# Kernel tuning notes

Measured on AMD Instinct MI355X. Metric: run time of the kernel, lower is better.

The kernel has to match this reference:

```python
import jax, jax.numpy as jnp
import numpy as np

EPS = 0.1          # entropic regularization (init eps)
MAX_ITER = 20      # Sinkhorn iterations (init max_iter)
THRESH = 0.1       # convergence threshold on err (from torch source)
COS_EPS = 1e-8     # CosineSimilarity eps


def setup_inputs() -> dict:
    key = jax.random.key(0)
    kx, ky = jax.random.split(key)
    B, N, M, D = 4, 1024, 1024, 512
    x = jax.random.normal(kx, (B, N, D), dtype=jnp.float32)
    y = jax.random.normal(ky, (B, M, D), dtype=jnp.float32)
    nu = jnp.full((B, M), 1.0 / M, dtype=jnp.float32)  # target marginal
    return {"x": x, "y": y, "nu": nu}


def _cost_matrix(x, y):
    # C_ij = 1 - cos(x_i, y_j), with torch CosineSimilarity eps semantics
    dot = jnp.einsum("bnd,bmd->bnm", x, y)
    nx = jnp.linalg.norm(x, axis=-1)  # [B, N]
    ny = jnp.linalg.norm(y, axis=-1)  # [B, M]
    denom = jnp.maximum(nx[:, :, None] * ny[:, None, :], COS_EPS)
    return 1.0 - dot / denom  # [B, N, M]


def reference(x, y, nu):
    C = _cost_matrix(x, y)  # [B, N, M]
    B, N, _ = C.shape
    log_mu = jnp.log(jnp.full((B, N), 1.0 / N, dtype=C.dtype) + 1e-8)  # [B, N]
    log_nu = jnp.log(nu + 1e-8)  # [B, M]

    def Mmat(u, v):
        # M_ij = (-C_ij + u_i + v_j) / eps
        return (-C + u[:, :, None] + v[:, None, :]) / EPS

    def step(carry, _):
        u, v, done = carry
        u_new = EPS * (log_mu - jax.scipy.special.logsumexp(Mmat(u, v), axis=-1)) + u
        v_new = EPS * (log_nu - jax.scipy.special.logsumexp(Mmat(u_new, v), axis=-2)) + v
        err = jnp.abs(u_new - u).sum(-1).mean()
        # freeze updates after convergence (emulates the host-side break)
        u2 = jnp.where(done, u, u_new)
        v2 = jnp.where(done, v, v_new)
        return (u2, v2, done | (err < THRESH)), None

    u0 = jnp.zeros_like(log_mu)
    v0 = jnp.zeros_like(log_nu)
    (u, v, _), _ = jax.lax.scan(step, (u0, v0, jnp.array(False)), None, length=MAX_ITER)

    pi = jnp.exp(Mmat(u, v))  # transport plan [B, N, M]
    cost = jnp.sum(pi * C, axis=(-2, -1))  # [B]  (reduction='none')
    return cost
```

## Files before the change

### kernel.cpp

```cpp
#include <hip/hip_runtime.h>
#include <math.h>

#define EPS      0.1f
#define INV_EPS  10.0f
#define THRESH   0.1f
#define MAX_IT   20

#define BB 4
#define NN 1024
#define MM 1024
#define DD 512

#define MU_P (1.0f / 1024.0f + 1e-8f)

#define GBLK 128
#define TBLK 512

#define OFF_K    ((size_t)0)
#define OFF_XB   ((size_t)2097152)
#define OFF_YB   ((size_t)3145728)
#define OFF_NX   ((size_t)4194304)
#define OFF_NY   (OFF_NX + 4096)
#define OFF_NUP  (OFF_NY + 4096)
#define OFF_CS   (OFF_NUP + 4096)
#define OFF_FLG  (OFF_CS + 12288)

#define GLDA 40

typedef __bf16 bf16x8 __attribute__((ext_vector_type(8)));
typedef float f32x4 __attribute__((ext_vector_type(4)));
typedef unsigned long long u64;

__device__ __forceinline__ float wave_reduce_sum(float x) {
#pragma unroll
  for (int off = 32; off > 0; off >>= 1) x += __shfl_xor(x, off, 64);
  return x;
}

__device__ __forceinline__ uint pk2(float a, float b) {
  __bf16 ha = (__bf16)a, hb = (__bf16)b;
  return (uint)*(ushort*)&ha | ((uint)*(ushort*)&hb << 16);
}

__global__ void __launch_bounds__(256) prep_kernel(const float* __restrict__ x,
                                                   const float* __restrict__ y,
                                                   ushort* __restrict__ xb,
                                                   ushort* __restrict__ yb,
                                                   float* __restrict__ nx,
                                                   float* __restrict__ ny,
                                                   const float* __restrict__ nu,
                                                   float* nup, float* colsum,
                                                   int* flagsi, float* out) {
  const int tid = threadIdx.x;
  int gt = blockIdx.x * 256 + tid;
  if (gt < BB * MM) {
    nup[gt] = nu[gt] + 1e-8f;
    colsum[4096 + gt] = 0.f;
  }
  if (gt < 512) flagsi[gt] = 0;
  if (gt < BB) out[gt] = 0.f;

  const int w = tid >> 6, lane = tid & 63;
  const int r = blockIdx.x * 4 + w;
  const bool isx = (r < BB * NN);
  const float* src = isx ? (x + (size_t)r * DD)
                         : (y + (size_t)(r - BB * NN) * DD);
  ushort* dst = isx ? (xb + (size_t)r * DD)
                    : (yb + (size_t)(r - BB * NN) * DD);
  const float4* s4 = (const float4*)src;
  float4 a = s4[lane * 2];
  float4 b = s4[lane * 2 + 1];
  float ss = a.x * a.x + a.y * a.y + a.z * a.z + a.w * a.w +
             b.x * b.x + b.y * b.y + b.z * b.z + b.w * b.w;
  uint4 pk = make_uint4(pk2(a.x, a.y), pk2(a.z, a.w), pk2(b.x, b.y), pk2(b.z, b.w));
  *(uint4*)(dst + lane * 8) = pk;
  ss = wave_reduce_sum(ss);
  if (lane == 0) {
    float n = sqrtf(ss);
    if (isx) nx[r] = n; else ny[r - BB * NN] = n;
  }
}

__global__ void __launch_bounds__(256) gemm_kernel(const ushort* __restrict__ xb,
                                                   const ushort* __restrict__ yb,
                                                   const float* __restrict__ nxg,
                                                   const float* __restrict__ nyg,
                                                   ushort* __restrict__ K) {
  __shared__ ushort Ah[128 * GLDA];
  __shared__ ushort Bh[128 * GLDA];
  __shared__ float s_nx[128], s_ny[128];

  const int b = blockIdx.z;
  const int i0 = blockIdx.y * 128;
  const int j0 = blockIdx.x * 128;
  const int t = threadIdx.x;
  const int w = t >> 6, lane = t & 63;
  const int m16 = lane & 15, q = lane >> 4;
  const int wm = (w & 1) * 64, wn = (w >> 1) * 64;

  const int srow = t >> 1;
  const int soff = (t & 1) * 16;

  const ushort* xrow = xb + ((size_t)b * NN + i0 + srow) * DD + soff;
  const ushort* yrow = yb + ((size_t)b * MM + j0 + srow) * DD + soff;

  f32x4 acc[4][4];
#pragma unroll
  for (int mi = 0; mi < 4; ++mi)
#pragma unroll
    for (int ni = 0; ni < 4; ++ni) acc[mi][ni] = (f32x4)0.f;

  for (int k0 = 0; k0 < DD; k0 += 32) {
    uint4 av0 = *(const uint4*)(xrow + k0);
    uint4 av1 = *(const uint4*)(xrow + k0 + 8);
    uint4 bv0 = *(const uint4*)(yrow + k0);
    uint4 bv1 = *(const uint4*)(yrow + k0 + 8);
    __syncthreads();
    *(uint4*)&Ah[srow * GLDA + soff] = av0;
    *(uint4*)&Ah[srow * GLDA + soff + 8] = av1;
    *(uint4*)&Bh[srow * GLDA + soff] = bv0;
    *(uint4*)&Bh[srow * GLDA + soff + 8] = bv1;
    __syncthreads();

    bf16x8 ahf[4], bhf[4];
#pragma unroll
    for (int mi = 0; mi < 4; ++mi)
      ahf[mi] = *(const bf16x8*)&Ah[(wm + mi * 16 + m16) * GLDA + q * 8];
#pragma unroll
    for (int ni = 0; ni < 4; ++ni)
      bhf[ni] = *(const bf16x8*)&Bh[(wn + ni * 16 + m16) * GLDA + q * 8];
#pragma unroll
    for (int mi = 0; mi < 4; ++mi)
#pragma unroll
      for (int ni = 0; ni < 4; ++ni)
        acc[mi][ni] = __builtin_amdgcn_mfma_f32_16x16x32_bf16(ahf[mi], bhf[ni], acc[mi][ni], 0, 0, 0);
  }

  if (t < 128) s_nx[t] = nxg[b * NN + i0 + t];
  else s_ny[t - 128] = nyg[b * MM + j0 + t - 128];
  __syncthreads();

#pragma unroll
  for (int mi = 0; mi < 4; ++mi)
#pragma unroll
    for (int ni = 0; ni < 4; ++ni)
#pragma unroll
      for (int r = 0; r < 4; ++r) {
        const int m = wm + mi * 16 + q * 4 + r;
        const int n = wn + ni * 16 + m16;
        float den = fmaxf(s_nx[m] * s_ny[n], 1e-8f);
        float cv = 1.0f - acc[mi][ni][r] / den;
        float kf = __expf(-cv * INV_EPS);
        __bf16 hb = (__bf16)kf;
        K[((size_t)b * NN + i0 + m) * MM + j0 + n] = *(ushort*)&hb;
      }
}

__device__ __forceinline__ void unpack8(uint4 k, float* kf) {
  kf[0] = __uint_as_float(k.x << 16);
  kf[1] = __uint_as_float(k.x & 0xffff0000u);
  kf[2] = __uint_as_float(k.y << 16);
  kf[3] = __uint_as_float(k.y & 0xffff0000u);
  kf[4] = __uint_as_float(k.z << 16);
  kf[5] = __uint_as_float(k.z & 0xffff0000u);
  kf[6] = __uint_as_float(k.w << 16);
  kf[7] = __uint_as_float(k.w & 0xffff0000u);
}

__global__ void __launch_bounds__(TBLK) sinkhorn_kernel(
    const ushort* __restrict__ K, float* __restrict__ colsum,
    const float* __restrict__ nup, u64* __restrict__ flags,
    float* __restrict__ out) {
  const int tid = threadIdx.x;
  const int bid = blockIdx.x;
  const int lane = tid & 63;
  const int w = tid >> 6;
  const int b = bid >> 5;
  const int rbase = (bid & 31) * 32;

  __shared__ float swv[1024];
  __shared__ float spart[8][1024];
  __shared__ float s_red;
  __shared__ int s_conv;

  const float eps_log_mu = EPS * __logf(MU_P);
  float u_prev[4] = {0.f, 0.f, 0.f, 0.f};
  float wu_reg[4] = {0.f, 0.f, 0.f, 0.f};
  int T = 0;

  for (int it = 0; it < MAX_IT; ++it) {
    const int genv = it + 1;
    if (tid == 0) s_red = 0.f;
    if (it == 0) {
      swv[tid] = 1.f;
      swv[tid + 512] = 1.f;
    } else {
      const float* cs = colsum + (it % 3) * 4096 + b * MM;
      float c0 = __hip_atomic_load(cs + tid, __ATOMIC_RELAXED, __HIP_MEMORY_SCOPE_AGENT);
      float c1 = __hip_atomic_load(cs + tid + 512, __ATOMIC_RELAXED, __HIP_MEMORY_SCOPE_AGENT);
      swv[tid] = nup[b * MM + tid] / c0;
      swv[tid + 512] = nup[b * MM + tid + 512] / c1;
    }
    __syncthreads();

    float wvr[16];
    {
      const float4* wp = (const float4*)swv;
      *(float4*)&wvr[0] = wp[lane * 2];
      *(float4*)&wvr[4] = wp[lane * 2 + 1];
      *(float4*)&wvr[8] = wp[128 + lane * 2];
      *(float4*)&wvr[12] = wp[129 + lane * 2];
    }
    float creg[16];
#pragma unroll
    for (int t2 = 0; t2 < 16; ++t2) creg[t2] = 0.f;

    uint4 kq[4][2];
#pragma unroll
    for (int rr = 0; rr < 4; ++rr) {
      const uint4* kp = (const uint4*)(K + ((size_t)b * NN + rbase + w * 4 + rr) * MM);
      kq[rr][0] = kp[lane];
      kq[rr][1] = kp[lane + 64];
    }

    float werr = 0.f;
#pragma unroll
    for (int rr = 0; rr < 4; ++rr) {
      float kf[16];
      unpack8(kq[rr][0], kf);
      unpack8(kq[rr][1], kf + 8);
      float s = 0.f;
#pragma unroll
      for (int t2 = 0; t2 < 16; ++t2) s = fmaf(kf[t2], wvr[t2], s);
      s = wave_reduce_sum(s);
      float unv = eps_log_mu - EPS * __logf(s);
      werr += fabsf(unv - u_prev[rr]);
      u_prev[rr] = unv;
      float wu = MU_P / s;
      wu_reg[rr] = wu;
#pragma unroll
      for (int t2 = 0; t2 < 16; ++t2) creg[t2] = fmaf(wu, kf[t2], creg[t2]);
    }
    if (lane == 0) atomicAdd(&s_red, werr);

    {
      float* pr = &spart[w][0];
      *(float4*)&pr[lane * 8] = *(float4*)&creg[0];
      *(float4*)&pr[lane * 8 + 4] = *(float4*)&creg[4];
      *(float4*)&pr[512 + lane * 8] = *(float4*)&creg[8];
      *(float4*)&pr[512 + lane * 8 + 4] = *(float4*)&creg[12];
    }
    __syncthreads();

    {
      float* csn = colsum + ((it + 1) % 3) * 4096 + b * MM;
      const int j0 = tid * 2;
      float s0 = 0.f, s1 = 0.f;
#pragma unroll
      for (int ww = 0; ww < 8; ++ww) {
        float2 p = *(const float2*)&spart[ww][j0];
        s0 += p.x;
        s1 += p.y;
      }
      unsafeAtomicAdd(&csn[j0], s0);
      unsafeAtomicAdd(&csn[j0 + 1], s1);
      if (tid < 32) {
        float* csz = colsum + ((it + 2) % 3) * 4096;
        __hip_atomic_store(&csz[bid * 32 + tid], 0.f, __ATOMIC_RELAXED, __HIP_MEMORY_SCOPE_AGENT);
      }
    }

    asm volatile("s_waitcnt vmcnt(0)" ::: "memory");
    __syncthreads();
    if (tid == 0) {
      u64 f = ((u64)(uint)genv << 32) | (u64)__float_as_uint(s_red);
      __hip_atomic_store(&flags[(genv & 1) * GBLK + bid], f, __ATOMIC_RELAXED, __HIP_MEMORY_SCOPE_AGENT);
    }
    if (tid < 64) {
      const u64* fl = flags + (genv & 1) * GBLK;
      u64 f0, f1;
      for (;;) {
        f0 = __hip_atomic_load(fl + tid, __ATOMIC_RELAXED, __HIP_MEMORY_SCOPE_AGENT);
        f1 = __hip_atomic_load(fl + tid + 64, __ATOMIC_RELAXED, __HIP_MEMORY_SCOPE_AGENT);
        if (__all(((f0 >> 32) >= (u64)genv) && ((f1 >> 32) >= (u64)genv))) break;
        __builtin_amdgcn_s_sleep(1);
      }
      float e = __uint_as_float((uint)f0) + __uint_as_float((uint)f1);
      e = wave_reduce_sum(e);
      if (tid == 0) s_conv = (e * (1.0f / (float)BB) < THRESH) ? 1 : 0;
    }
    __syncthreads();
    T = it;
    if (s_conv) break;
  }

  {
    const float* cs = colsum + ((T + 1) % 3) * 4096 + b * MM;
    float c0 = __hip_atomic_load(cs + tid, __ATOMIC_RELAXED, __HIP_MEMORY_SCOPE_AGENT);
    float c1 = __hip_atomic_load(cs + tid + 512, __ATOMIC_RELAXED, __HIP_MEMORY_SCOPE_AGENT);
    swv[tid] = nup[b * MM + tid] / c0;
    swv[tid + 512] = nup[b * MM + tid + 512] / c1;
  }
  if (tid == 0) s_red = 0.f;
  __syncthreads();

  float wvr[16];
  {
    const float4* wp = (const float4*)swv;
    *(float4*)&wvr[0] = wp[lane * 2];
    *(float4*)&wvr[4] = wp[lane * 2 + 1];
    *(float4*)&wvr[8] = wp[128 + lane * 2];
    *(float4*)&wvr[12] = wp[129 + lane * 2];
  }

  float wcost = 0.f;
#pragma unroll
  for (int rr = 0; rr < 4; ++rr) {
    const int r = rbase + w * 4 + rr;
    const uint4* kp = (const uint4*)(K + ((size_t)b * NN + r) * MM);
    uint4 k0 = kp[lane], k1 = kp[lane + 64];
    float kf[16];
    unpack8(k0, kf);
    unpack8(k1, kf + 8);
    float s = 0.f;
#pragma unroll
    for (int t2 = 0; t2 < 16; ++t2)
      s = fmaf(kf[t2] * wvr[t2], -EPS * __logf(kf[t2]), s);
    s = wave_reduce_sum(s) * wu_reg[rr];
    if (lane == 0) wcost += s;
  }
  if (lane == 0) atomicAdd(&s_red, wcost);
  __syncthreads();
  if (tid == 0) atomicAdd(out + b, s_red);
}

extern "C" void kernel_launch(void* const* d_in, const int* in_sizes, int n_in,
                              void* d_out, int out_size, void* d_ws, size_t ws_size,
                              hipStream_t stream) {
  const float* x = (const float*)d_in[0];
  const float* y = (const float*)d_in[1];
  const float* nu = (const float*)d_in[2];
  float* out = (float*)d_out;
  float* ws = (float*)d_ws;

  ushort* K = (ushort*)(ws + OFF_K);
  ushort* xb = (ushort*)(ws + OFF_XB);
  ushort* yb = (ushort*)(ws + OFF_YB);
  float* nx = ws + OFF_NX;
  float* ny = ws + OFF_NY;
  float* nup = ws + OFF_NUP;
  float* cs = ws + OFF_CS;
  u64* flg = (u64*)(ws + OFF_FLG);

  prep_kernel<<<2048, 256, 0, stream>>>(x, y, xb, yb, nx, ny, nu, nup, cs, (int*)flg, out);
  gemm_kernel<<<dim3(8, 8, 4), 256, 0, stream>>>(xb, yb, nx, ny, K);

  void* args[] = {(void*)&K, (void*)&cs, (void*)&nup, (void*)&flg, (void*)&out};
  hipLaunchCooperativeKernel(reinterpret_cast<void*>(&sinkhorn_kernel),
                             dim3(GBLK), dim3(TBLK), args, 0, stream);
}
```

Baseline: 126.3 us.

## Keep K tile resident in registers across Sinkhorn iterations; halve GEMM N-tile

The Sinkhorn kernel now loads and unpacks its K rows once into a 64-float register array before the iteration loop, and reuses them in every iteration and in the final cost pass. This removes repeated global/L2 reads of K on each of the 20 iterations. Launch bounds are adjusted to hint register allocation, which risks spilling given the larger live set. Separately, the GEMM tile is changed from 128x128 to 128x64, doubling the grid to 512 blocks so more CUs are busy, at the cost of reloading A tiles more often.

Result: no change. 127.5 us (+1.0%).

```diff
diff --git a/kernel.cpp b/kernel.cpp
--- a/kernel.cpp
+++ b/kernel.cpp
@@ -87,63 +87,61 @@
                                                    const float* __restrict__ nyg,
                                                    ushort* __restrict__ K) {
   __shared__ ushort Ah[128 * GLDA];
-  __shared__ ushort Bh[128 * GLDA];
-  __shared__ float s_nx[128], s_ny[128];
+  __shared__ ushort Bh[64 * GLDA];
+  __shared__ float s_nx[128], s_ny[64];
 
   const int b = blockIdx.z;
   const int i0 = blockIdx.y * 128;
-  const int j0 = blockIdx.x * 128;
+  const int j0 = blockIdx.x * 64;
   const int t = threadIdx.x;
   const int w = t >> 6, lane = t & 63;
   const int m16 = lane & 15, q = lane >> 4;
-  const int wm = (w & 1) * 64, wn = (w >> 1) * 64;
-
-  const int srow = t >> 1;
-  const int soff = (t & 1) * 16;
-
-  const ushort* xrow = xb + ((size_t)b * NN + i0 + srow) * DD + soff;
-  const ushort* yrow = yb + ((size_t)b * MM + j0 + srow) * DD + soff;
-
-  f32x4 acc[4][4];
+  const int wm = (w & 1) * 64, wn = (w >> 1) * 32;
+
+  const int srA = t >> 1, soA = (t & 1) * 16;
+  const int srB = t >> 2, soB = (t & 3) * 8;
+
+  const ushort* xrow = xb + ((size_t)b * NN + i0 + srA) * DD + soA;
+  const ushort* yrow = yb + ((size_t)b * MM + j0 + srB) * DD + soB;
+
+  f32x4 acc[4][2];
 #pragma unroll
   for (int mi = 0; mi < 4; ++mi)
 #pragma unroll
-    for (int ni = 0; ni < 4; ++ni) acc[mi][ni] = (f32x4)0.f;
+    for (int ni = 0; ni < 2; ++ni) acc[mi][ni] = (f32x4)0.f;
 
   for (int k0 = 0; k0 < DD; k0 += 32) {
     uint4 av0 = *(const uint4*)(xrow + k0);
     uint4 av1 = *(const uint4*)(xrow + k0 + 8);
     uint4 bv0 = *(const uint4*)(yrow + k0);
-    uint4 bv1 = *(const uint4*)(yrow + k0 + 8);
-    __syncthreads();
-    *(uint4*)&Ah[srow * GLDA + soff] = av0;
-    *(uint4*)&Ah[srow * GLDA + soff + 8] = av1;
-    *(uint4*)&Bh[srow * GLDA + soff] = bv0;
-    *(uint4*)&Bh[srow * GLDA + soff + 8] = bv1;
-    __syncthreads();
-
-    bf16x8 ahf[4], bhf[4];
+    __syncthreads();
+    *(uint4*)&Ah[srA * GLDA + soA] = av0;
+    *(uint4*)&Ah[srA * GLDA + soA + 8] = av1;
+    *(uint4*)&Bh[srB * GLDA + soB] = bv0;
+    __syncthreads();
+
+    bf16x8 ahf[4], bhf[2];
 #pragma unroll
     for (int mi = 0; mi < 4; ++mi)
       ahf[mi] = *(const bf16x8*)&Ah[(wm + mi * 16 + m16) * GLDA + q * 8];
 #pragma unroll
-    for (int ni = 0; ni < 4; ++ni)
+    for (int ni = 0; ni < 2; ++ni)
       bhf[ni] = *(const bf16x8*)&Bh[(wn + ni * 16 + m16) * GLDA + q * 8];
 #pragma unroll
     for (int mi = 0; mi < 4; ++mi)
 #pragma unroll
-      for (int ni = 0; ni < 4; ++ni)
+      for (int ni = 0; ni < 2; ++ni)
         acc[mi][ni] = __builtin_amdgcn_mfma_f32_16x16x32_bf16(ahf[mi], bhf[ni], acc[mi][ni], 0, 0, 0);
   }
 
   if (t < 128) s_nx[t] = nxg[b * NN + i0 + t];
-  else s_ny[t - 128] = nyg[b * MM + j0 + t - 128];
+  else if (t < 192) s_ny[t - 128] = nyg[b * MM + j0 + t - 128];
   __syncthreads();
 
 #pragma unroll
   for (int mi = 0; mi < 4; ++mi)
 #pragma unroll
-    for (int ni = 0; ni < 4; ++ni)
+    for (int ni = 0; ni < 2; ++ni)
 #pragma unroll
       for (int r = 0; r < 4; ++r) {
         const int m = wm + mi * 16 + q * 4 + r;
@@ -167,7 +165,7 @@
   kf[7] = __uint_as_float(k.w & 0xffff0000u);
 }
 
-__global__ void __launch_bounds__(TBLK) sinkhorn_kernel(
+__global__ void __launch_bounds__(TBLK, 2) sinkhorn_kernel(
     const ushort* __restrict__ K, float* __restrict__ colsum,
     const float* __restrict__ nup, u64* __restrict__ flags,
     float* __restrict__ out) {
@@ -187,6 +185,16 @@
   float u_prev[4] = {0.f, 0.f, 0.f, 0.f};
   float wu_reg[4] = {0.f, 0.f, 0.f, 0.f};
   int T = 0;
+
+  float kf[4][16];
+#pragma unroll
+  for (int rr = 0; rr < 4; ++rr) {
+    const uint4* kp = (const uint4*)(K + ((size_t)b * NN + rbase + w * 4 + rr) * MM);
+    uint4 k0 = kp[lane];
+    uint4 k1 = kp[lane + 64];
+    unpack8(k0, kf[rr]);
+    unpack8(k1, kf[rr] + 8);
+  }
 
   for (int it = 0; it < MAX_IT; ++it) {
     const int genv = it + 1;
@@ -215,23 +223,12 @@
 #pragma unroll
     for (int t2 = 0; t2 < 16; ++t2) creg[t2] = 0.f;
 
-    uint4 kq[4][2];
+    float werr = 0.f;
 #pragma unroll
     for (int rr = 0; rr < 4; ++rr) {
-      const uint4* kp = (const uint4*)(K + ((size_t)b * NN + rbase + w * 4 + rr) * MM);
-      kq[rr][0] = kp[lane];
-      kq[rr][1] = kp[lane + 64];
-    }
-
-    float werr = 0.f;
-#pragma unroll
-    for (int rr = 0; rr < 4; ++rr) {
-      float kf[16];
-      unpack8(kq[rr][0], kf);
-      unpack8(kq[rr][1], kf + 8);
       float s = 0.f;
 #pragma unroll
-      for (int t2 = 0; t2 < 16; ++t2) s = fmaf(kf[t2], wvr[t2], s);
+      for (int t2 = 0; t2 < 16; ++t2) s = fmaf(kf[rr][t2], wvr[t2], s);
       s = wave_reduce_sum(s);
       float unv = eps_log_mu - EPS * __logf(s);
       werr += fabsf(unv - u_prev[rr]);
@@ -239,7 +236,7 @@
       float wu = MU_P / s;
       wu_reg[rr] = wu;
 #pragma unroll
-      for (int t2 = 0; t2 < 16; ++t2) creg[t2] = fmaf(wu, kf[t2], creg[t2]);
+      for (int t2 = 0; t2 < 16; ++t2) creg[t2] = fmaf(wu, kf[rr][t2], creg[t2]);
     }
     if (lane == 0) atomicAdd(&s_red, werr);
 
@@ -316,16 +313,10 @@
   float wcost = 0.f;
 #pragma unroll
   for (int rr = 0; rr < 4; ++rr) {
-    const int r = rbase + w * 4 + rr;
-    const uint4* kp = (const uint4*)(K + ((size_t)b * NN + r) * MM);
-    uint4 k0 = kp[lane], k1 = kp[lane + 64];
-    float kf[16];
-    unpack8(k0, kf);
-    unpack8(k1, kf + 8);
     float s = 0.f;
 #pragma unroll
     for (int t2 = 0; t2 < 16; ++t2)
-      s = fmaf(kf[t2] * wvr[t2], -EPS * __logf(kf[t2]), s);
+      s = fmaf(kf[rr][t2] * wvr[t2], -EPS * __logf(kf[rr][t2]), s);
     s = wave_reduce_sum(s) * wu_reg[rr];
     if (lane == 0) wcost += s;
   }
@@ -353,7 +344,7 @@
   u64* flg = (u64*)(ws + OFF_FLG);
 
   prep_kernel<<<2048, 256, 0, stream>>>(x, y, xb, yb, nx, ny, nu, nup, cs, (int*)flg, out);
-  gemm_kernel<<<dim3(8, 8, 4), 256, 0, stream>>>(xb, yb, nx, ny, K);
+  gemm_kernel<<<dim3(16, 8, 4), 256, 0, stream>>>(xb, yb, nx, ny, K);
 
   void* args[] = {(void*)&K, (void*)&cs, (void*)&nup, (void*)&flg, (void*)&out};
   hipLaunchCooperativeKernel(reinterpret_cast<void*>(&sinkhorn_kernel),
```
